# Kernel tuning notes

Hardware: AMD Instinct MI355X
Metric: run time of the kernel (lower is better)

The kernel has to match this reference:

```python
import jax, jax.numpy as jnp
import numpy as np

Z_SIZE, KEY_SIZE, HID = 128, 256, 512
NEG = -1e9


def setup_inputs() -> dict:
    key = jax.random.key(0)
    ks = jax.random.split(key, 8)
    B, T, H, W, Y = 512, 32, 32, 32, 4
    D = H * W
    g = lambda k, shape, s: jax.random.normal(k, shape, jnp.float32) * s
    return {
        "x_seq": jax.random.normal(ks[0], (B, T, H, W), jnp.float32),
        # Encoder (conv encoder stand-in: flatten -> MLP -> z_size)
        "enc_w1": g(ks[1], (D, HID), 0.03),
        "enc_b1": jnp.zeros((HID,), jnp.float32),
        "enc_w2": g(ks[2], (HID, Z_SIZE), 0.05),
        "enc_b2": jnp.zeros((Z_SIZE,), jnp.float32),
        # LSTM input kernel (recurrent kernel unused: h_prev is always 0)
        "lstm_Wx": g(ks[3], (KEY_SIZE + 1, 4 * HID), 0.05),
        "lstm_b": jnp.zeros((4 * HID,), jnp.float32),
        "keyw_W": g(ks[4], (HID, KEY_SIZE), 0.05),
        "keyw_b": jnp.zeros((KEY_SIZE,), jnp.float32),
        "g_W": g(ks[5], (HID, 1), 0.05),
        "g_b": jnp.zeros((1,), jnp.float32),
        "y_W": g(ks[6], (HID, Y), 0.05),
        "y_b": jnp.zeros((Y,), jnp.float32),
        "conf_gain": jnp.float32(1.0),
        "conf_bias": jnp.float32(0.0),
    }


def reference(x_seq, enc_w1, enc_b1, enc_w2, enc_b2, lstm_Wx, lstm_b,
              keyw_W, keyw_b, g_W, g_b, y_W, y_b, conf_gain, conf_bias):
    B, T = x_seq.shape[0], x_seq.shape[1]
    Y = y_b.shape[0]
    dt = x_seq.dtype

    # Encode all frames at once: (B, T, Z)
    x_flat = x_seq.reshape(B, T, -1)
    z_seq = jax.nn.relu(x_flat @ enc_w1 + enc_b1) @ enc_w2 + enc_b2
    # Pad with the zero z_t used at the final step t == T  -> (B, T+1, Z)
    z_pad = jnp.concatenate([z_seq, jnp.zeros((B, 1, Z_SIZE), dt)], axis=1)

    def lstm_step(x):  # single keras LSTM step from zero state (h=c=0)
        gates = x @ lstm_Wx + lstm_b
        i, f, c, o = jnp.split(gates, 4, axis=-1)  # keras gate order i,f,c,o
        c_new = jax.nn.sigmoid(i) * jnp.tanh(c)     # f*c_prev = 0
        return jax.nn.sigmoid(o) * jnp.tanh(c_new)

    slot_idx = jnp.arange(T + 1)

    def step(carry, t):
        key_r, M_k, M_v, _ = carry
        z_t = z_pad[:, t]                       # (B, Z)
        h = lstm_step(key_r)                    # (B, HID)
        key_w = h @ keyw_W + keyw_b             # (B, KEY)
        gate = jax.nn.sigmoid(h @ g_W + g_b)    # (B, 1)
        y_lin = h @ y_W + y_b                   # (B, Y)

        # Content-based read over memory slots written so far (slots < t)
        scores = jnp.einsum('bz,btz->bt', z_t, M_v)          # (B, T+1)
        valid = (slot_idx < t)[None, :]
        w_k = jax.nn.softmax(jnp.where(valid, scores, NEG), axis=1)
        c_k = jax.nn.sigmoid(scores * conf_gain + conf_bias)  # (B, T+1)
        Mkc = jnp.concatenate([M_k, c_k[..., None]], axis=-1)  # (B, T+1, KEY+1)
        key_r_new = gate * jnp.einsum('bt,btk->bk', w_k, Mkc)
        key_r_new = jnp.where(t == 0, jnp.zeros_like(key_r_new), key_r_new)

        # Memory write (append == write into preallocated slot t)
        M_k = M_k.at[:, t].set(key_w)
        M_v = M_v.at[:, t].set(z_t)
        return (key_r_new, M_k, M_v, y_lin), None

    init = (jnp.zeros((B, KEY_SIZE + 1), dt),
            jnp.zeros((B, T + 1, KEY_SIZE), dt),
            jnp.zeros((B, T + 1, Z_SIZE), dt),
            jnp.zeros((B, Y), dt))
    (_, _, _, y_pred_linear), _ = jax.lax.scan(step, init, jnp.arange(T + 1))
    y_pred = jnp.argmax(y_pred_linear, axis=1)
    return y_pred_linear, y_pred
```

## Files before the change

### kernel.cpp

```cpp
#include <hip/hip_runtime.h>
#include <math.h>

__device__ __forceinline__ float sigf(float x) { return 1.0f / (1.0f + expf(-x)); }
__device__ __forceinline__ float4 f4fma(float s, float4 b, float4 a) {
  return make_float4(fmaf(s, b.x, a.x), fmaf(s, b.y, a.y), fmaf(s, b.z, a.z), fmaf(s, b.w, a.w));
}
__device__ __forceinline__ void wave_red2(float4& v) {
  v.x += __shfl_xor(v.x, 16); v.y += __shfl_xor(v.y, 16);
  v.z += __shfl_xor(v.z, 16); v.w += __shfl_xor(v.w, 16);
  v.x += __shfl_xor(v.x, 32); v.y += __shfl_xor(v.y, 32);
  v.z += __shfl_xor(v.z, 32); v.w += __shfl_xor(v.w, 32);
}

__global__ __launch_bounds__(256) void k_gemm1(const float* __restrict__ X,
                                               const float* __restrict__ W,
                                               const float* __restrict__ Bv,
                                               float* __restrict__ C)
{
  const int K = 1024, N = 512;
  __shared__ float As[16][132];
  __shared__ float Bs[16][132];
  int tid = threadIdx.x;
  int bm = blockIdx.x >> 2;
  int bn = blockIdx.x & 3;
  int tx = tid & 15, ty = tid >> 4;
  int xr = tid & 127, xc8 = (tid >> 7) * 8;
  int wk = tid >> 4, wc = (tid & 15) * 8;
  const float* Xb = X + (size_t)(bm * 128 + xr) * K;
  const float* Wb = W + bn * 128 + wc;
  float acc[8][8];
#pragma unroll
  for (int i = 0; i < 8; i++)
#pragma unroll
    for (int j = 0; j < 8; j++) acc[i][j] = 0.f;

  for (int k0 = 0; k0 < K; k0 += 16) {
    float4 a0 = *(const float4*)(Xb + k0 + xc8);
    float4 a1 = *(const float4*)(Xb + k0 + xc8 + 4);
    float4 b0 = *(const float4*)(W + (size_t)(k0 + wk) * N + bn * 128 + wc);
    float4 b1 = *(const float4*)(W + (size_t)(k0 + wk) * N + bn * 128 + wc + 4);
    As[xc8 + 0][xr] = a0.x; As[xc8 + 1][xr] = a0.y;
    As[xc8 + 2][xr] = a0.z; As[xc8 + 3][xr] = a0.w;
    As[xc8 + 4][xr] = a1.x; As[xc8 + 5][xr] = a1.y;
    As[xc8 + 6][xr] = a1.z; As[xc8 + 7][xr] = a1.w;
    *(float4*)(&Bs[wk][wc]) = b0;
    *(float4*)(&Bs[wk][wc + 4]) = b1;
    __syncthreads();
#pragma unroll
    for (int kk = 0; kk < 16; kk++) {
      float a[8], b[8];
      *(float4*)(a)     = *(const float4*)(&As[kk][ty * 8]);
      *(float4*)(a + 4) = *(const float4*)(&As[kk][ty * 8 + 4]);
      *(float4*)(b)     = *(const float4*)(&Bs[kk][tx * 4]);
      *(float4*)(b + 4) = *(const float4*)(&Bs[kk][64 + tx * 4]);
#pragma unroll
      for (int i = 0; i < 8; i++)
#pragma unroll
        for (int j = 0; j < 8; j++) acc[i][j] = fmaf(a[i], b[j], acc[i][j]);
    }
    __syncthreads();
  }
  int crow0 = bm * 128 + ty * 8;
  int ccolA = bn * 128 + tx * 4;
  int ccolB = bn * 128 + 64 + tx * 4;
  float4 bvA = *(const float4*)(Bv + ccolA);
  float4 bvB = *(const float4*)(Bv + ccolB);
#pragma unroll
  for (int i = 0; i < 8; i++) {
    float4 vA = make_float4(acc[i][0] + bvA.x, acc[i][1] + bvA.y,
                            acc[i][2] + bvA.z, acc[i][3] + bvA.w);
    float4 vB = make_float4(acc[i][4] + bvB.x, acc[i][5] + bvB.y,
                            acc[i][6] + bvB.z, acc[i][7] + bvB.w);
    vA.x = vA.x > 0.f ? vA.x : 0.f; vA.y = vA.y > 0.f ? vA.y : 0.f;
    vA.z = vA.z > 0.f ? vA.z : 0.f; vA.w = vA.w > 0.f ? vA.w : 0.f;
    vB.x = vB.x > 0.f ? vB.x : 0.f; vB.y = vB.y > 0.f ? vB.y : 0.f;
    vB.z = vB.z > 0.f ? vB.z : 0.f; vB.w = vB.w > 0.f ? vB.w : 0.f;
    *(float4*)(&C[(size_t)(crow0 + i) * N + ccolA]) = vA;
    *(float4*)(&C[(size_t)(crow0 + i) * N + ccolB]) = vB;
  }
}

__global__ __launch_bounds__(256) void k_gemm2(const float* __restrict__ A,
                                               const float* __restrict__ W,
                                               const float* __restrict__ Bv,
                                               float* __restrict__ zp)
{
  const int K = 512, N = 128;
  __shared__ float As[8][132];
  __shared__ float Bs[8][132];
  int tid = threadIdx.x;
  int bm = blockIdx.x;
  int tx = tid & 15, ty = tid >> 4;
  int arow = tid >> 1, acol4 = (tid & 1) * 4;
  int bkk = tid >> 5, bn4 = (tid & 31) * 4;
  const float* Ab = A + (size_t)(bm * 128) * K;
  float acc[8][8];
#pragma unroll
  for (int i = 0; i < 8; i++)
#pragma unroll
    for (int j2 = 0; j2 < 8; j2++) acc[i][j2] = 0.f;
  for (int k0 = 0; k0 < K; k0 += 8) {
    float4 av = *(const float4*)(Ab + (size_t)arow * K + k0 + acol4);
    float4 bv = *(const float4*)(W + (size_t)(k0 + bkk) * N + bn4);
    As[acol4 + 0][arow] = av.x;
    As[acol4 + 1][arow] = av.y;
    As[acol4 + 2][arow] = av.z;
    As[acol4 + 3][arow] = av.w;
    *(float4*)(&Bs[bkk][bn4]) = bv;
    __syncthreads();
#pragma unroll
    for (int kk = 0; kk < 8; kk++) {
      float a[8], b[8];
      *(float4*)(a)     = *(const float4*)(&As[kk][ty * 8]);
      *(float4*)(a + 4) = *(const float4*)(&As[kk][ty * 8 + 4]);
      *(float4*)(b)     = *(const float4*)(&Bs[kk][tx * 8]);
      *(float4*)(b + 4) = *(const float4*)(&Bs[kk][tx * 8 + 4]);
#pragma unroll
      for (int i = 0; i < 8; i++)
#pragma unroll
        for (int j2 = 0; j2 < 8; j2++) acc[i][j2] = fmaf(a[i], b[j2], acc[i][j2]);
    }
    __syncthreads();
  }
  int ccol0 = tx * 8;
#pragma unroll
  for (int i = 0; i < 8; i++) {
    int r = bm * 128 + ty * 8 + i;
    int b = r >> 5, tt = r & 31;
#pragma unroll
    for (int j2 = 0; j2 < 8; j2++) {
      zp[(size_t)b * (33 * 128) + tt * 128 + ccol0 + j2] = acc[i][j2] + Bv[ccol0 + j2];
    }
  }
}

__global__ __launch_bounds__(256) void k_gram(const float* __restrict__ zp,
                                              float* __restrict__ warr,
                                              float* __restrict__ wc,
                                              const float* __restrict__ cgp,
                                              const float* __restrict__ cbp)
{
  __shared__ float zl[32][128];
  __shared__ float sg[32][32];
  int b = blockIdx.x, tid = threadIdx.x;
  const float* zb = zp + (size_t)b * (33 * 128);
  for (int i = tid; i < 32 * 128; i += 256) (&zl[0][0])[i] = zb[i];
  __syncthreads();
  for (int p = tid; p < 496; p += 256) {
    int t = 1;
    while (p >= t * (t + 1) / 2) t++;
    int tp = p - t * (t - 1) / 2;
    const float* za = &zl[t][0];
    const float* zc = &zl[tp][0];
    float s = 0.f;
#pragma unroll 4
    for (int c = 0; c < 128; c += 4) {
      s += za[c] * zc[c] + za[c + 1] * zc[c + 1] + za[c + 2] * zc[c + 2] + za[c + 3] * zc[c + 3];
    }
    sg[t][tp] = s;
  }
  __syncthreads();
  if (tid >= 1 && tid < 32) {
    int t = tid;
    float cg = cgp[0], cb = cbp[0];
    float m = -3.0e38f;
    for (int tp = 0; tp < t; tp++) m = fmaxf(m, sg[t][tp]);
    float se = 0.f;
    for (int tp = 0; tp < t; tp++) se += expf(sg[t][tp] - m);
    float inv = 1.0f / se;
    float wcs = 0.f;
    for (int tp = 0; tp < t; tp++) {
      float s = sg[t][tp];
      float w = expf(s - m) * inv;
      warr[(size_t)b * 1024 + t * 32 + tp] = w;
      wcs = fmaf(w, sigf(fmaf(s, cg, cb)), wcs);
    }
    wc[b * 32 + t] = wcs;
  }
}

__global__ __launch_bounds__(256) void k_gates(const float* __restrict__ Wx,
                                               const float* __restrict__ lb,
                                               const float* __restrict__ keyrT,
                                               float* __restrict__ h, int t)
{
  __shared__ float smem[6656];
  float* As = smem;
  float* Bs = smem + 640;
  float* Rb = smem;
  const int tid = threadIdx.x;
  const int rt = blockIdx.x >> 4;
  const int ct = blockIdx.x & 15;
  const int row0 = rt * 16;
  const int hc0 = ct * 32;

  if (t > 0) {
    const int ksub = tid >> 4;
    const int pos = tid & 15;
    const int rg = pos >> 3;
    const int cg = pos & 7;
    float4 aI[8], aC[8], aO[8];
#pragma unroll
    for (int r = 0; r < 8; r++) {
      aI[r] = make_float4(0.f, 0.f, 0.f, 0.f);
      aC[r] = make_float4(0.f, 0.f, 0.f, 0.f);
      aO[r] = make_float4(0.f, 0.f, 0.f, 0.f);
    }
    for (int c = 0; c < 8; ++c) {
      const int k0 = c * 32;
      if (c) __syncthreads();
      if (tid < 128) {
        const int kkA = tid >> 2, lA = (tid & 3) * 4;
        *(float4*)&As[kkA * 20 + lA] =
            *(const float4*)&keyrT[(size_t)(k0 + kkA) * 512 + row0 + lA];
      }
      {
        const int kkB = tid >> 3, lB = (tid & 7) * 4;
        const float* wrow = Wx + (size_t)(k0 + kkB) * 2048;
        *(float4*)&Bs[kkB * 100 + lB]      = *(const float4*)(wrow + hc0 + lB);
        *(float4*)&Bs[kkB * 100 + 32 + lB] = *(const float4*)(wrow + 1024 + hc0 + lB);
        *(float4*)&Bs[kkB * 100 + 64 + lB] = *(const float4*)(wrow + 1536 + hc0 + lB);
      }
      __syncthreads();
#pragma unroll
      for (int i = 0; i < 2; ++i) {
        const int kk = ksub * 2 + i;
        float a8[8];
        *(float4*)&a8[0] = *(const float4*)&As[kk * 20 + rg * 8];
        *(float4*)&a8[4] = *(const float4*)&As[kk * 20 + rg * 8 + 4];
        float4 bI = *(const float4*)&Bs[kk * 100 + cg * 4];
        float4 bC = *(const float4*)&Bs[kk * 100 + 32 + cg * 4];
        float4 bO = *(const float4*)&Bs[kk * 100 + 64 + cg * 4];
#pragma unroll
        for (int r = 0; r < 8; r++) {
          float a = a8[r];
          aI[r] = f4fma(a, bI, aI[r]);
          aC[r] = f4fma(a, bC, aC[r]);
          aO[r] = f4fma(a, bO, aO[r]);
        }
      }
    }
    if (ksub == 0) {
      float a8[8];
      *(float4*)&a8[0] = *(const float4*)&keyrT[(size_t)256 * 512 + row0 + rg * 8];
      *(float4*)&a8[4] = *(const float4*)&keyrT[(size_t)256 * 512 + row0 + rg * 8 + 4];
      const float* wrow = Wx + (size_t)256 * 2048;
      float4 bI = *(const float4*)(wrow + hc0 + cg * 4);
      float4 bC = *(const float4*)(wrow + 1024 + hc0 + cg * 4);
      float4 bO = *(const float4*)(wrow + 1536 + hc0 + cg * 4);
#pragma unroll
      for (int r = 0; r < 8; r++) {
        float a = a8[r];
        aI[r] = f4fma(a, bI, aI[r]);
        aC[r] = f4fma(a, bC, aC[r]);
        aO[r] = f4fma(a, bO, aO[r]);
      }
    }
#pragma unroll
    for (int r = 0; r < 8; r++) { wave_red2(aI[r]); wave_red2(aC[r]); wave_red2(aO[r]); }
    __syncthreads();
    {
      const int wave = tid >> 6, lane = tid & 63;
      if (lane < 16) {
        float* w = &Rb[wave * 1600 + lane * 100];
#pragma unroll
        for (int r = 0; r < 8; r++) {
          *(float4*)&w[r * 12 + 0] = aI[r];
          *(float4*)&w[r * 12 + 4] = aC[r];
          *(float4*)&w[r * 12 + 8] = aO[r];
        }
      }
    }
    __syncthreads();
    {
      const int r = tid >> 4;
      const int hc2 = (tid & 15) * 2;
      const int p = (r >> 3) * 8 + (hc2 >> 2);
      const int base = p * 100 + (r & 7) * 12;
      const int off = hc2 & 3;
      float sI0 = Rb[base + off]     + Rb[1600 + base + off]     + Rb[3200 + base + off]     + Rb[4800 + base + off];
      float sI1 = Rb[base + off + 1] + Rb[1600 + base + off + 1] + Rb[3200 + base + off + 1] + Rb[4800 + base + off + 1];
      float sC0 = Rb[base + 4 + off]     + Rb[1600 + base + 4 + off]     + Rb[3200 + base + 4 + off]     + Rb[4800 + base + 4 + off];
      float sC1 = Rb[base + 4 + off + 1] + Rb[1600 + base + 4 + off + 1] + Rb[3200 + base + 4 + off + 1] + Rb[4800 + base + 4 + off + 1];
      float sO0 = Rb[base + 8 + off]     + Rb[1600 + base + 8 + off]     + Rb[3200 + base + 8 + off]     + Rb[4800 + base + 8 + off];
      float sO1 = Rb[base + 8 + off + 1] + Rb[1600 + base + 8 + off + 1] + Rb[3200 + base + 8 + off + 1] + Rb[4800 + base + 8 + off + 1];
      float iv0 = sI0 + lb[hc0 + hc2],        iv1 = sI1 + lb[hc0 + hc2 + 1];
      float cv0 = sC0 + lb[1024 + hc0 + hc2], cv1 = sC1 + lb[1024 + hc0 + hc2 + 1];
      float ov0 = sO0 + lb[1536 + hc0 + hc2], ov1 = sO1 + lb[1536 + hc0 + hc2 + 1];
      float h0 = sigf(ov0) * tanhf(sigf(iv0) * tanhf(cv0));
      float h1 = sigf(ov1) * tanhf(sigf(iv1) * tanhf(cv1));
      *(float2*)&h[(size_t)(row0 + r) * 512 + hc0 + hc2] = make_float2(h0, h1);
    }
  } else {
    const int r = tid >> 4;
    const int hc2 = (tid & 15) * 2;
    float iv0 = lb[hc0 + hc2],        iv1 = lb[hc0 + hc2 + 1];
    float cv0 = lb[1024 + hc0 + hc2], cv1 = lb[1024 + hc0 + hc2 + 1];
    float ov0 = lb[1536 + hc0 + hc2], ov1 = lb[1536 + hc0 + hc2 + 1];
    float h0 = sigf(ov0) * tanhf(sigf(iv0) * tanhf(cv0));
    float h1 = sigf(ov1) * tanhf(sigf(iv1) * tanhf(cv1));
    *(float2*)&h[(size_t)(row0 + r) * 512 + hc0 + hc2] = make_float2(h0, h1);
  }
}

__global__ __launch_bounds__(256) void k_update(const float* __restrict__ h,
                                                const float* __restrict__ kW,
                                                const float* __restrict__ kb,
                                                const float* __restrict__ gW,
                                                const float* __restrict__ gb,
                                                const float* __restrict__ warr,
                                                const float* __restrict__ wc,
                                                float* __restrict__ Mk,
                                                float* __restrict__ keyrT, int t)
{
  __shared__ float smem[10640];
  float* hs  = smem;
  float* gWs = smem + 8256;
  float* wws = smem + 8768;
  float* gsh = smem + 9344;
  float* kWs = smem + 9360;
  float* Rb  = smem + 9360;
  const int tid = threadIdx.x;
  const int rt = blockIdx.x >> 4;
  const int ct = blockIdx.x & 15;
  const int row0 = rt * 16;
  const int c0 = ct * 16;

  {
    const int r = tid >> 4, seg = tid & 15;
    const float* hrow = h + (size_t)(row0 + r) * 512 + seg * 32;
    float* hd = hs + r * 516 + seg * 32;
#pragma unroll
    for (int q = 0; q < 8; ++q) {
      const int qp = ((q + seg) & 7) * 4;
      *(float4*)&hd[qp] = *(const float4*)&hrow[qp];
    }
    if (tid < 128) *(float4*)&gWs[tid * 4] = *(const float4*)&gW[tid * 4];
    wws[r * 36 + seg]      = (seg < t)      ? warr[(size_t)(row0 + r) * 1024 + t * 32 + seg] : 0.f;
    wws[r * 36 + 16 + seg] = (16 + seg < t) ? warr[(size_t)(row0 + r) * 1024 + t * 32 + 16 + seg] : 0.f;
  }
  __syncthreads();

  const int ksub = tid >> 4, pu = tid & 15, rgu = pu >> 2, cgu = pu & 3;
  float4 au[4];
#pragma unroll
  for (int r = 0; r < 4; r++) au[r] = make_float4(0.f, 0.f, 0.f, 0.f);
  for (int c = 0; c < 16; ++c) {
    if (c) __syncthreads();
    if (tid < 128) {
      const int kkW = tid >> 2, lW = (tid & 3) * 4;
      *(float4*)&kWs[kkW * 20 + lW] =
          *(const float4*)&kW[(size_t)(c * 32 + kkW) * 256 + c0 + lW];
    }
    __syncthreads();
#pragma unroll
    for (int i = 0; i < 2; ++i) {
      const int kk = ksub * 2 + i;
      float4 b4 = *(const float4*)&kWs[kk * 20 + cgu * 4];
      const int kidx = c * 32 + kk;
#pragma unroll
      for (int jj = 0; jj < 4; ++jj) {
        float a = hs[(rgu * 4 + jj) * 516 + kidx];
        au[jj] = f4fma(a, b4, au[jj]);
      }
    }
  }
#pragma unroll
  for (int r = 0; r < 4; r++) wave_red2(au[r]);
  __syncthreads();
  {
    const int wave = tid >> 6, lane = tid & 63;
    if (lane < 16) {
      float* w = &Rb[wave * 320 + lane * 20];
#pragma unroll
      for (int r = 0; r < 4; r++) *(float4*)&w[r * 4] = au[r];
    }
  }
  __syncthreads();
  {
    const int r = tid >> 4, cc = tid & 15;
    const int p = (r >> 2) * 4 + (cc >> 2);
    const int e = p * 20 + (r & 3) * 4 + (cc & 3);
    float v = Rb[e] + Rb[320 + e] + Rb[640 + e] + Rb[960 + e];
    Mk[(size_t)(row0 + r) * 8192 + t * 256 + c0 + cc] = v + kb[c0 + cc];
  }
  {
    const int r = tid >> 4, seg = tid & 15;
    const float* hp = &hs[r * 516 + seg * 32];
    const float* gp = &gWs[seg * 32];
    float s = 0.f;
#pragma unroll 8
    for (int j = 0; j < 32; ++j) s = fmaf(hp[j], gp[j], s);
    s += __shfl_xor(s, 1); s += __shfl_xor(s, 2);
    s += __shfl_xor(s, 4); s += __shfl_xor(s, 8);
    if (seg == 0) gsh[r] = sigf(s + gb[0]);
  }
  __syncthreads();
  {
    const int r = tid >> 4, cc = tid & 15;
    const int row = row0 + r;
    if (t == 0) {
      keyrT[(size_t)(c0 + cc) * 512 + row] = 0.f;
      if (ct == 0 && cc == 0) keyrT[(size_t)256 * 512 + row] = 0.f;
    } else {
      float a = 0.f;
      const float* mkb = Mk + (size_t)row * 8192 + c0 + cc;
      const float* wp = &wws[r * 36];
      for (int tp = 0; tp < t; ++tp) a = fmaf(wp[tp], mkb[tp * 256], a);
      float g = gsh[r];
      keyrT[(size_t)(c0 + cc) * 512 + row] = g * a;
      if (ct == 0 && cc == 0)
        keyrT[(size_t)256 * 512 + row] = g * wc[row * 32 + t];
    }
  }
}

__global__ __launch_bounds__(256) void k_y(const float* __restrict__ h,
                                           const float* __restrict__ yW,
                                           const float* __restrict__ yb,
                                           float* __restrict__ out)
{
  int tid = threadIdx.x;
  int wave = tid >> 6, lane = tid & 63;
  int row = blockIdx.x * 4 + wave;
  float a0 = 0.f, a1 = 0.f, a2 = 0.f, a3 = 0.f;
  for (int k = lane; k < 512; k += 64) {
    float hv = h[(size_t)row * 512 + k];
    float4 w4 = *(const float4*)(yW + k * 4);
    a0 = fmaf(hv, w4.x, a0);
    a1 = fmaf(hv, w4.y, a1);
    a2 = fmaf(hv, w4.z, a2);
    a3 = fmaf(hv, w4.w, a3);
  }
#pragma unroll
  for (int off = 32; off > 0; off >>= 1) {
    a0 += __shfl_xor(a0, off);
    a1 += __shfl_xor(a1, off);
    a2 += __shfl_xor(a2, off);
    a3 += __shfl_xor(a3, off);
  }
  if (lane == 0) {
    a0 += yb[0]; a1 += yb[1]; a2 += yb[2]; a3 += yb[3];
    out[row * 4 + 0] = a0;
    out[row * 4 + 1] = a1;
    out[row * 4 + 2] = a2;
    out[row * 4 + 3] = a3;
    int bi = 0; float bv = a0;
    if (a1 > bv) { bv = a1; bi = 1; }
    if (a2 > bv) { bv = a2; bi = 2; }
    if (a3 > bv) { bv = a3; bi = 3; }
    out[2048 + row] = (float)bi;
  }
}

extern "C" void kernel_launch(void* const* d_in, const int* in_sizes, int n_in,
                              void* d_out, int out_size, void* d_ws, size_t ws_size,
                              hipStream_t stream)
{
  const float* x  = (const float*)d_in[0];
  const float* w1 = (const float*)d_in[1];
  const float* b1 = (const float*)d_in[2];
  const float* w2 = (const float*)d_in[3];
  const float* b2 = (const float*)d_in[4];
  const float* Wx = (const float*)d_in[5];
  const float* lb = (const float*)d_in[6];
  const float* kW = (const float*)d_in[7];
  const float* kb = (const float*)d_in[8];
  const float* gW = (const float*)d_in[9];
  const float* gb = (const float*)d_in[10];
  const float* yW = (const float*)d_in[11];
  const float* yb = (const float*)d_in[12];
  const float* cg = (const float*)d_in[13];
  const float* cb = (const float*)d_in[14];
  float* out = (float*)d_out;
  char* ws = (char*)d_ws;
  float* C1    = (float*)(ws);
  float* Mk    = (float*)(ws);
  float* warr  = (float*)(ws + 16777216);
  float* wcb   = (float*)(ws + 18874368);
  float* keyrT = (float*)(ws + 18939904);
  float* h     = (float*)(ws + 19466240);
  float* zp    = (float*)(ws + 33554432);

  hipLaunchKernelGGL(k_gemm1, dim3(512), dim3(256), 0, stream, x, w1, b1, C1);
  hipLaunchKernelGGL(k_gemm2, dim3(128), dim3(256), 0, stream, C1, w2, b2, zp);
  hipLaunchKernelGGL(k_gram, dim3(512), dim3(256), 0, stream, zp, warr, wcb, cg, cb);
  for (int t = 0; t <= 32; t++) {
    hipLaunchKernelGGL(k_gates, dim3(512), dim3(256), 0, stream, Wx, lb, keyrT, h, t);
    if (t < 32) {
      hipLaunchKernelGGL(k_update, dim3(512), dim3(256), 0, stream,
                         h, kW, kb, gW, gb, warr, wcb, Mk, keyrT, t);
    }
  }
  hipLaunchKernelGGL(k_y, dim3(128), dim3(256), 0, stream, h, yW, yb, out);
}
```

Baseline: 1.320 ms.

## Fuse per-step gate and memory-update kernels into one split-K step kernel with atomics

Merges the LSTM gate kernel and the memory-update kernel into a single per-timestep kernel, halving launches in the recurrent loop. The key-write projection is split across column tiles and accumulated with atomicAdd into Mk and a gate accumulator, and the gated read is deferred to the next step through double-buffered partial buffers. The encoder GEMMs also get smaller tiles so more blocks are launched. The cost is float atomics with nondeterministic summation order, extra initialisation of Mk and gacc, and more complex cross-step dependencies.

```diff
diff --git a/kernel.cpp b/kernel.cpp
--- a/kernel.cpp
+++ b/kernel.cpp
@@ -18,63 +18,65 @@
                                                float* __restrict__ C)
 {
   const int K = 1024, N = 512;
-  __shared__ float As[16][132];
+  __shared__ float As[16][68];
   __shared__ float Bs[16][132];
-  int tid = threadIdx.x;
-  int bm = blockIdx.x >> 2;
-  int bn = blockIdx.x & 3;
-  int tx = tid & 15, ty = tid >> 4;
-  int xr = tid & 127, xc8 = (tid >> 7) * 8;
-  int wk = tid >> 4, wc = (tid & 15) * 8;
-  const float* Xb = X + (size_t)(bm * 128 + xr) * K;
-  const float* Wb = W + bn * 128 + wc;
-  float acc[8][8];
-#pragma unroll
-  for (int i = 0; i < 8; i++)
+  const int tid = threadIdx.x;
+  const int bm = blockIdx.x >> 2;
+  const int bn = blockIdx.x & 3;
+  const int ty = tid >> 4, tx = tid & 15;
+  const int ar = tid & 63, ac4 = (tid >> 6) * 4;
+  const int bk = tid >> 4, bc8 = (tid & 15) * 8;
+  const float* Xb = X + (size_t)(bm * 64 + ar) * K;
+  float acc[4][8];
+#pragma unroll
+  for (int i = 0; i < 4; i++)
 #pragma unroll
     for (int j = 0; j < 8; j++) acc[i][j] = 0.f;
 
   for (int k0 = 0; k0 < K; k0 += 16) {
-    float4 a0 = *(const float4*)(Xb + k0 + xc8);
-    float4 a1 = *(const float4*)(Xb + k0 + xc8 + 4);
-    float4 b0 = *(const float4*)(W + (size_t)(k0 + wk) * N + bn * 128 + wc);
-    float4 b1 = *(const float4*)(W + (size_t)(k0 + wk) * N + bn * 128 + wc + 4);
-    As[xc8 + 0][xr] = a0.x; As[xc8 + 1][xr] = a0.y;
-    As[xc8 + 2][xr] = a0.z; As[xc8 + 3][xr] = a0.w;
-    As[xc8 + 4][xr] = a1.x; As[xc8 + 5][xr] = a1.y;
-    As[xc8 + 6][xr] = a1.z; As[xc8 + 7][xr] = a1.w;
-    *(float4*)(&Bs[wk][wc]) = b0;
-    *(float4*)(&Bs[wk][wc + 4]) = b1;
+    float4 av = *(const float4*)(Xb + k0 + ac4);
+    float4 b0 = *(const float4*)(W + (size_t)(k0 + bk) * N + bn * 128 + bc8);
+    float4 b1 = *(const float4*)(W + (size_t)(k0 + bk) * N + bn * 128 + bc8 + 4);
+    As[ac4 + 0][ar] = av.x; As[ac4 + 1][ar] = av.y;
+    As[ac4 + 2][ar] = av.z; As[ac4 + 3][ar] = av.w;
+    *(float4*)(&Bs[bk][bc8]) = b0;
+    *(float4*)(&Bs[bk][bc8 + 4]) = b1;
     __syncthreads();
 #pragma unroll
     for (int kk = 0; kk < 16; kk++) {
-      float a[8], b[8];
-      *(float4*)(a)     = *(const float4*)(&As[kk][ty * 8]);
-      *(float4*)(a + 4) = *(const float4*)(&As[kk][ty * 8 + 4]);
-      *(float4*)(b)     = *(const float4*)(&Bs[kk][tx * 4]);
-      *(float4*)(b + 4) = *(const float4*)(&Bs[kk][64 + tx * 4]);
-#pragma unroll
-      for (int i = 0; i < 8; i++)
-#pragma unroll
-        for (int j = 0; j < 8; j++) acc[i][j] = fmaf(a[i], b[j], acc[i][j]);
-    }
-    __syncthreads();
-  }
-  int crow0 = bm * 128 + ty * 8;
-  int ccolA = bn * 128 + tx * 4;
-  int ccolB = bn * 128 + 64 + tx * 4;
+      float4 a = *(const float4*)(&As[kk][ty * 4]);
+      float4 bA = *(const float4*)(&Bs[kk][tx * 4]);
+      float4 bB = *(const float4*)(&Bs[kk][64 + tx * 4]);
+      float ar4[4] = {a.x, a.y, a.z, a.w};
+#pragma unroll
+      for (int i = 0; i < 4; i++) {
+        acc[i][0] = fmaf(ar4[i], bA.x, acc[i][0]);
+        acc[i][1] = fmaf(ar4[i], bA.y, acc[i][1]);
+        acc[i][2] = fmaf(ar4[i], bA.z, acc[i][2]);
+        acc[i][3] = fmaf(ar4[i], bA.w, acc[i][3]);
+        acc[i][4] = fmaf(ar4[i], bB.x, acc[i][4]);
+        acc[i][5] = fmaf(ar4[i], bB.y, acc[i][5]);
+        acc[i][6] = fmaf(ar4[i], bB.z, acc[i][6]);
+        acc[i][7] = fmaf(ar4[i], bB.w, acc[i][7]);
+      }
+    }
+    __syncthreads();
+  }
+  const int crow0 = bm * 64 + ty * 4;
+  const int ccolA = bn * 128 + tx * 4;
+  const int ccolB = ccolA + 64;
   float4 bvA = *(const float4*)(Bv + ccolA);
   float4 bvB = *(const float4*)(Bv + ccolB);
 #pragma unroll
-  for (int i = 0; i < 8; i++) {
+  for (int i = 0; i < 4; i++) {
     float4 vA = make_float4(acc[i][0] + bvA.x, acc[i][1] + bvA.y,
                             acc[i][2] + bvA.z, acc[i][3] + bvA.w);
     float4 vB = make_float4(acc[i][4] + bvB.x, acc[i][5] + bvB.y,
                             acc[i][6] + bvB.z, acc[i][7] + bvB.w);
-    vA.x = vA.x > 0.f ? vA.x : 0.f; vA.y = vA.y > 0.f ? vA.y : 0.f;
-    vA.z = vA.z > 0.f ? vA.z : 0.f; vA.w = vA.w > 0.f ? vA.w : 0.f;
-    vB.x = vB.x > 0.f ? vB.x : 0.f; vB.y = vB.y > 0.f ? vB.y : 0.f;
-    vB.z = vB.z > 0.f ? vB.z : 0.f; vB.w = vB.w > 0.f ? vB.w : 0.f;
+    vA.x = fmaxf(vA.x, 0.f); vA.y = fmaxf(vA.y, 0.f);
+    vA.z = fmaxf(vA.z, 0.f); vA.w = fmaxf(vA.w, 0.f);
+    vB.x = fmaxf(vB.x, 0.f); vB.y = fmaxf(vB.y, 0.f);
+    vB.z = fmaxf(vB.z, 0.f); vB.w = fmaxf(vB.w, 0.f);
     *(float4*)(&C[(size_t)(crow0 + i) * N + ccolA]) = vA;
     *(float4*)(&C[(size_t)(crow0 + i) * N + ccolB]) = vB;
   }
@@ -86,51 +88,57 @@
                                                float* __restrict__ zp)
 {
   const int K = 512, N = 128;
-  __shared__ float As[8][132];
-  __shared__ float Bs[8][132];
-  int tid = threadIdx.x;
-  int bm = blockIdx.x;
-  int tx = tid & 15, ty = tid >> 4;
-  int arow = tid >> 1, acol4 = (tid & 1) * 4;
-  int bkk = tid >> 5, bn4 = (tid & 31) * 4;
-  const float* Ab = A + (size_t)(bm * 128) * K;
-  float acc[8][8];
-#pragma unroll
-  for (int i = 0; i < 8; i++)
-#pragma unroll
-    for (int j2 = 0; j2 < 8; j2++) acc[i][j2] = 0.f;
-  for (int k0 = 0; k0 < K; k0 += 8) {
-    float4 av = *(const float4*)(Ab + (size_t)arow * K + k0 + acol4);
-    float4 bv = *(const float4*)(W + (size_t)(k0 + bkk) * N + bn4);
-    As[acol4 + 0][arow] = av.x;
-    As[acol4 + 1][arow] = av.y;
-    As[acol4 + 2][arow] = av.z;
-    As[acol4 + 3][arow] = av.w;
-    *(float4*)(&Bs[bkk][bn4]) = bv;
-    __syncthreads();
-#pragma unroll
-    for (int kk = 0; kk < 8; kk++) {
-      float a[8], b[8];
-      *(float4*)(a)     = *(const float4*)(&As[kk][ty * 8]);
-      *(float4*)(a + 4) = *(const float4*)(&As[kk][ty * 8 + 4]);
-      *(float4*)(b)     = *(const float4*)(&Bs[kk][tx * 8]);
-      *(float4*)(b + 4) = *(const float4*)(&Bs[kk][tx * 8 + 4]);
-#pragma unroll
-      for (int i = 0; i < 8; i++)
-#pragma unroll
-        for (int j2 = 0; j2 < 8; j2++) acc[i][j2] = fmaf(a[i], b[j2], acc[i][j2]);
-    }
-    __syncthreads();
-  }
-  int ccol0 = tx * 8;
-#pragma unroll
-  for (int i = 0; i < 8; i++) {
-    int r = bm * 128 + ty * 8 + i;
+  __shared__ float As[16][36];
+  __shared__ float Bs[16][132];
+  const int tid = threadIdx.x;
+  const int bm = blockIdx.x;
+  const int ty = tid >> 4, tx = tid & 15;
+  const int ar = tid & 31, ac4 = ((tid >> 5) & 3) * 4;
+  const int bk = tid >> 4, bc8 = (tid & 15) * 8;
+  float acc[2][8];
+#pragma unroll
+  for (int i = 0; i < 2; i++)
+#pragma unroll
+    for (int j = 0; j < 8; j++) acc[i][j] = 0.f;
+
+  for (int k0 = 0; k0 < K; k0 += 16) {
+    if (tid < 128) {
+      float4 av = *(const float4*)(A + (size_t)(bm * 32 + ar) * K + k0 + ac4);
+      As[ac4 + 0][ar] = av.x; As[ac4 + 1][ar] = av.y;
+      As[ac4 + 2][ar] = av.z; As[ac4 + 3][ar] = av.w;
+    }
+    *(float4*)(&Bs[bk][bc8]) = *(const float4*)(W + (size_t)(k0 + bk) * N + bc8);
+    *(float4*)(&Bs[bk][bc8 + 4]) = *(const float4*)(W + (size_t)(k0 + bk) * N + bc8 + 4);
+    __syncthreads();
+#pragma unroll
+    for (int kk = 0; kk < 16; kk++) {
+      float a0 = As[kk][ty * 2], a1 = As[kk][ty * 2 + 1];
+      float4 bA = *(const float4*)(&Bs[kk][tx * 4]);
+      float4 bB = *(const float4*)(&Bs[kk][64 + tx * 4]);
+      acc[0][0] = fmaf(a0, bA.x, acc[0][0]); acc[0][1] = fmaf(a0, bA.y, acc[0][1]);
+      acc[0][2] = fmaf(a0, bA.z, acc[0][2]); acc[0][3] = fmaf(a0, bA.w, acc[0][3]);
+      acc[0][4] = fmaf(a0, bB.x, acc[0][4]); acc[0][5] = fmaf(a0, bB.y, acc[0][5]);
+      acc[0][6] = fmaf(a0, bB.z, acc[0][6]); acc[0][7] = fmaf(a0, bB.w, acc[0][7]);
+      acc[1][0] = fmaf(a1, bA.x, acc[1][0]); acc[1][1] = fmaf(a1, bA.y, acc[1][1]);
+      acc[1][2] = fmaf(a1, bA.z, acc[1][2]); acc[1][3] = fmaf(a1, bA.w, acc[1][3]);
+      acc[1][4] = fmaf(a1, bB.x, acc[1][4]); acc[1][5] = fmaf(a1, bB.y, acc[1][5]);
+      acc[1][6] = fmaf(a1, bB.z, acc[1][6]); acc[1][7] = fmaf(a1, bB.w, acc[1][7]);
+    }
+    __syncthreads();
+  }
+  const int ccolA = tx * 4, ccolB = ccolA + 64;
+  float4 bvA = *(const float4*)(Bv + ccolA);
+  float4 bvB = *(const float4*)(Bv + ccolB);
+#pragma unroll
+  for (int i = 0; i < 2; i++) {
+    int r = bm * 32 + ty * 2 + i;
     int b = r >> 5, tt = r & 31;
-#pragma unroll
-    for (int j2 = 0; j2 < 8; j2++) {
-      zp[(size_t)b * (33 * 128) + tt * 128 + ccol0 + j2] = acc[i][j2] + Bv[ccol0 + j2];
-    }
+    float4 vA = make_float4(acc[i][0] + bvA.x, acc[i][1] + bvA.y,
+                            acc[i][2] + bvA.z, acc[i][3] + bvA.w);
+    float4 vB = make_float4(acc[i][4] + bvB.x, acc[i][5] + bvB.y,
+                            acc[i][6] + bvB.z, acc[i][7] + bvB.w);
+    *(float4*)(&zp[(size_t)b * 4096 + tt * 128 + ccolA]) = vA;
+    *(float4*)(&zp[(size_t)b * 4096 + tt * 128 + ccolB]) = vB;
   }
 }
 
@@ -138,13 +146,18 @@
                                               float* __restrict__ warr,
                                               float* __restrict__ wc,
                                               const float* __restrict__ cgp,
-                                              const float* __restrict__ cbp)
+                                              const float* __restrict__ cbp,
+                                              const float* __restrict__ kb,
+                                              float* __restrict__ Mk,
+                                              float* __restrict__ gacc)
 {
   __shared__ float zl[32][128];
   __shared__ float sg[32][32];
   int b = blockIdx.x, tid = threadIdx.x;
-  const float* zb = zp + (size_t)b * (33 * 128);
+  const float* zb = zp + (size_t)b * 4096;
   for (int i = tid; i < 32 * 128; i += 256) (&zl[0][0])[i] = zb[i];
+  Mk[(size_t)b * 8192 + tid] = kb[tid];
+  if (tid == 0) gacc[b * 32] = 0.f;
   __syncthreads();
   for (int p = tid; p < 496; p += 256) {
     int t = 1;
@@ -179,22 +192,47 @@
   }
 }
 
-__global__ __launch_bounds__(256) void k_gates(const float* __restrict__ Wx,
-                                               const float* __restrict__ lb,
-                                               const float* __restrict__ keyrT,
-                                               float* __restrict__ h, int t)
-{
-  __shared__ float smem[6656];
-  float* As = smem;
-  float* Bs = smem + 640;
-  float* Rb = smem;
+__global__ __launch_bounds__(256) void k_step(
+    const float* __restrict__ Wx, const float* __restrict__ lb,
+    const float* __restrict__ kW, const float* __restrict__ kb,
+    const float* __restrict__ gW, const float* __restrict__ gb,
+    const float* __restrict__ warr, const float* __restrict__ wc,
+    float* __restrict__ Mk, float* __restrict__ gacc,
+    const float* __restrict__ Pr, float* __restrict__ Pw,
+    float* __restrict__ h, int t)
+{
+  __shared__ float smem[9984];
+  float* As   = smem;
+  float* Bs   = smem + 5140;
+  float* Rb   = smem;
+  float* kWs  = smem;
+  float* hs   = smem + 8340;
+  float* wws  = smem + 8916;
+  float* gt16 = smem + 9428;
+  float* gsh  = smem + 9684;
+  float* Ptmp = smem + 9700;
   const int tid = threadIdx.x;
   const int rt = blockIdx.x >> 4;
   const int ct = blockIdx.x & 15;
   const int row0 = rt * 16;
   const int hc0 = ct * 32;
-
-  if (t > 0) {
+  const int c0 = ct * 16;
+
+  if (t >= 2) {
+    if (tid < 16) gsh[tid] = sigf(gacc[(row0 + tid) * 32 + (t - 1)] + gb[0]);
+    __syncthreads();
+    const int p16 = tid >> 4, r16 = tid & 15;
+    const float g = gsh[r16];
+#pragma unroll 4
+    for (int kg = 0; kg < 16; ++kg) {
+      const int k = kg * 16 + p16;
+      As[k * 20 + r16] = g * Pr[(size_t)k * 512 + row0 + r16];
+    }
+    if (p16 == 0) As[256 * 20 + r16] = g * wc[(row0 + r16) * 32 + (t - 1)];
+    __syncthreads();
+  }
+
+  if (t >= 2) {
     const int ksub = tid >> 4;
     const int pos = tid & 15;
     const int rg = pos >> 3;
@@ -207,16 +245,10 @@
       aO[r] = make_float4(0.f, 0.f, 0.f, 0.f);
     }
     for (int c = 0; c < 8; ++c) {
-      const int k0 = c * 32;
       if (c) __syncthreads();
-      if (tid < 128) {
-        const int kkA = tid >> 2, lA = (tid & 3) * 4;
-        *(float4*)&As[kkA * 20 + lA] =
-            *(const float4*)&keyrT[(size_t)(k0 + kkA) * 512 + row0 + lA];
-      }
       {
         const int kkB = tid >> 3, lB = (tid & 7) * 4;
-        const float* wrow = Wx + (size_t)(k0 + kkB) * 2048;
+        const float* wrow = Wx + (size_t)(c * 32 + kkB) * 2048;
         *(float4*)&Bs[kkB * 100 + lB]      = *(const float4*)(wrow + hc0 + lB);
         *(float4*)&Bs[kkB * 100 + 32 + lB] = *(const float4*)(wrow + 1024 + hc0 + lB);
         *(float4*)&Bs[kkB * 100 + 64 + lB] = *(const float4*)(wrow + 1536 + hc0 + lB);
@@ -225,9 +257,10 @@
 #pragma unroll
       for (int i = 0; i < 2; ++i) {
         const int kk = ksub * 2 + i;
+        const int kabs = c * 32 + kk;
         float a8[8];
-        *(float4*)&a8[0] = *(const float4*)&As[kk * 20 + rg * 8];
-        *(float4*)&a8[4] = *(const float4*)&As[kk * 20 + rg * 8 + 4];
+        *(float4*)&a8[0] = *(const float4*)&As[kabs * 20 + rg * 8];
+        *(float4*)&a8[4] = *(const float4*)&As[kabs * 20 + rg * 8 + 4];
         float4 bI = *(const float4*)&Bs[kk * 100 + cg * 4];
         float4 bC = *(const float4*)&Bs[kk * 100 + 32 + cg * 4];
         float4 bO = *(const float4*)&Bs[kk * 100 + 64 + cg * 4];
@@ -242,8 +275,8 @@
     }
     if (ksub == 0) {
       float a8[8];
-      *(float4*)&a8[0] = *(const float4*)&keyrT[(size_t)256 * 512 + row0 + rg * 8];
-      *(float4*)&a8[4] = *(const float4*)&keyrT[(size_t)256 * 512 + row0 + rg * 8 + 4];
+      *(float4*)&a8[0] = *(const float4*)&As[256 * 20 + rg * 8];
+      *(float4*)&a8[4] = *(const float4*)&As[256 * 20 + rg * 8 + 4];
       const float* wrow = Wx + (size_t)256 * 2048;
       float4 bI = *(const float4*)(wrow + hc0 + cg * 4);
       float4 bC = *(const float4*)(wrow + 1024 + hc0 + cg * 4);
@@ -289,128 +322,96 @@
       float ov0 = sO0 + lb[1536 + hc0 + hc2], ov1 = sO1 + lb[1536 + hc0 + hc2 + 1];
       float h0 = sigf(ov0) * tanhf(sigf(iv0) * tanhf(cv0));
       float h1 = sigf(ov1) * tanhf(sigf(iv1) * tanhf(cv1));
-      *(float2*)&h[(size_t)(row0 + r) * 512 + hc0 + hc2] = make_float2(h0, h1);
+      hs[r * 36 + hc2] = h0;
+      hs[r * 36 + hc2 + 1] = h1;
+      if (t == 32) *(float2*)&h[(size_t)(row0 + r) * 512 + hc0 + hc2] = make_float2(h0, h1);
     }
   } else {
     const int r = tid >> 4;
     const int hc2 = (tid & 15) * 2;
-    float iv0 = lb[hc0 + hc2],        iv1 = lb[hc0 + hc2 + 1];
-    float cv0 = lb[1024 + hc0 + hc2], cv1 = lb[1024 + hc0 + hc2 + 1];
-    float ov0 = lb[1536 + hc0 + hc2], ov1 = lb[1536 + hc0 + hc2 + 1];
-    float h0 = sigf(ov0) * tanhf(sigf(iv0) * tanhf(cv0));
-    float h1 = sigf(ov1) * tanhf(sigf(iv1) * tanhf(cv1));
-    *(float2*)&h[(size_t)(row0 + r) * 512 + hc0 + hc2] = make_float2(h0, h1);
-  }
-}
-
-__global__ __launch_bounds__(256) void k_update(const float* __restrict__ h,
-                                                const float* __restrict__ kW,
-                                                const float* __restrict__ kb,
-                                                const float* __restrict__ gW,
-                                                const float* __restrict__ gb,
-                                                const float* __restrict__ warr,
-                                                const float* __restrict__ wc,
-                                                float* __restrict__ Mk,
-                                                float* __restrict__ keyrT, int t)
-{
-  __shared__ float smem[10640];
-  float* hs  = smem;
-  float* gWs = smem + 8256;
-  float* wws = smem + 8768;
-  float* gsh = smem + 9344;
-  float* kWs = smem + 9360;
-  float* Rb  = smem + 9360;
-  const int tid = threadIdx.x;
-  const int rt = blockIdx.x >> 4;
-  const int ct = blockIdx.x & 15;
-  const int row0 = rt * 16;
-  const int c0 = ct * 16;
-
-  {
-    const int r = tid >> 4, seg = tid & 15;
-    const float* hrow = h + (size_t)(row0 + r) * 512 + seg * 32;
-    float* hd = hs + r * 516 + seg * 32;
-#pragma unroll
-    for (int q = 0; q < 8; ++q) {
-      const int qp = ((q + seg) & 7) * 4;
-      *(float4*)&hd[qp] = *(const float4*)&hrow[qp];
-    }
-    if (tid < 128) *(float4*)&gWs[tid * 4] = *(const float4*)&gW[tid * 4];
-    wws[r * 36 + seg]      = (seg < t)      ? warr[(size_t)(row0 + r) * 1024 + t * 32 + seg] : 0.f;
-    wws[r * 36 + 16 + seg] = (16 + seg < t) ? warr[(size_t)(row0 + r) * 1024 + t * 32 + 16 + seg] : 0.f;
+    float h0 = sigf(lb[1536 + hc0 + hc2])     * tanhf(sigf(lb[hc0 + hc2])     * tanhf(lb[1024 + hc0 + hc2]));
+    float h1 = sigf(lb[1536 + hc0 + hc2 + 1]) * tanhf(sigf(lb[hc0 + hc2 + 1]) * tanhf(lb[1024 + hc0 + hc2 + 1]));
+    hs[r * 36 + hc2] = h0;
+    hs[r * 36 + hc2 + 1] = h1;
   }
   __syncthreads();
 
-  const int ksub = tid >> 4, pu = tid & 15, rgu = pu >> 2, cgu = pu & 3;
-  float4 au[4];
-#pragma unroll
-  for (int r = 0; r < 4; r++) au[r] = make_float4(0.f, 0.f, 0.f, 0.f);
-  for (int c = 0; c < 16; ++c) {
-    if (c) __syncthreads();
-    if (tid < 128) {
-      const int kkW = tid >> 2, lW = (tid & 3) * 4;
-      *(float4*)&kWs[kkW * 20 + lW] =
-          *(const float4*)&kW[(size_t)(c * 32 + kkW) * 256 + c0 + lW];
-    }
-    __syncthreads();
-#pragma unroll
-    for (int i = 0; i < 2; ++i) {
-      const int kk = ksub * 2 + i;
-      float4 b4 = *(const float4*)&kWs[kk * 20 + cgu * 4];
-      const int kidx = c * 32 + kk;
-#pragma unroll
-      for (int jj = 0; jj < 4; ++jj) {
-        float a = hs[(rgu * 4 + jj) * 516 + kidx];
-        au[jj] = f4fma(a, b4, au[jj]);
-      }
-    }
-  }
-#pragma unroll
-  for (int r = 0; r < 4; r++) wave_red2(au[r]);
-  __syncthreads();
-  {
-    const int wave = tid >> 6, lane = tid & 63;
-    if (lane < 16) {
-      float* w = &Rb[wave * 320 + lane * 20];
-#pragma unroll
-      for (int r = 0; r < 4; r++) *(float4*)&w[r * 4] = au[r];
-    }
-  }
-  __syncthreads();
-  {
-    const int r = tid >> 4, cc = tid & 15;
-    const int p = (r >> 2) * 4 + (cc >> 2);
-    const int e = p * 20 + (r & 3) * 4 + (cc & 3);
-    float v = Rb[e] + Rb[320 + e] + Rb[640 + e] + Rb[960 + e];
-    Mk[(size_t)(row0 + r) * 8192 + t * 256 + c0 + cc] = v + kb[c0 + cc];
-  }
-  {
-    const int r = tid >> 4, seg = tid & 15;
-    const float* hp = &hs[r * 516 + seg * 32];
-    const float* gp = &gWs[seg * 32];
-    float s = 0.f;
-#pragma unroll 8
-    for (int j = 0; j < 32; ++j) s = fmaf(hp[j], gp[j], s);
-    s += __shfl_xor(s, 1); s += __shfl_xor(s, 2);
-    s += __shfl_xor(s, 4); s += __shfl_xor(s, 8);
-    if (seg == 0) gsh[r] = sigf(s + gb[0]);
-  }
-  __syncthreads();
-  {
-    const int r = tid >> 4, cc = tid & 15;
-    const int row = row0 + r;
-    if (t == 0) {
-      keyrT[(size_t)(c0 + cc) * 512 + row] = 0.f;
-      if (ct == 0 && cc == 0) keyrT[(size_t)256 * 512 + row] = 0.f;
-    } else {
-      float a = 0.f;
-      const float* mkb = Mk + (size_t)row * 8192 + c0 + cc;
-      const float* wp = &wws[r * 36];
-      for (int tp = 0; tp < t; ++tp) a = fmaf(wp[tp], mkb[tp * 256], a);
-      float g = gsh[r];
-      keyrT[(size_t)(c0 + cc) * 512 + row] = g * a;
-      if (ct == 0 && cc == 0)
-        keyrT[(size_t)256 * 512 + row] = g * wc[row * 32 + t];
+  if (t < 32) {
+    const int rC = tid >> 4, cb = tid & 15;
+    float4 a16[4];
+#pragma unroll
+    for (int j = 0; j < 4; j++) a16[j] = make_float4(0.f, 0.f, 0.f, 0.f);
+#pragma unroll
+    for (int half = 0; half < 2; ++half) {
+      __syncthreads();
+      {
+        const int rowW = tid >> 4;
+        const int cc4 = (tid & 15) * 4;
+#pragma unroll
+        for (int q = 0; q < 4; ++q) {
+          *(float4*)&kWs[rowW * 260 + cc4 + q * 64] =
+              *(const float4*)&kW[(size_t)(hc0 + half * 16 + rowW) * 256 + cc4 + q * 64];
+        }
+      }
+      __syncthreads();
+#pragma unroll
+      for (int kk = 0; kk < 16; ++kk) {
+        float a = hs[rC * 36 + half * 16 + kk];
+#pragma unroll
+        for (int j = 0; j < 4; ++j) {
+          float4 b = *(const float4*)&kWs[kk * 260 + j * 64 + cb * 4];
+          a16[j] = f4fma(a, b, a16[j]);
+        }
+      }
+    }
+    {
+      float* mkt = Mk + (size_t)(row0 + rC) * 8192 + t * 256;
+#pragma unroll
+      for (int j = 0; j < 4; ++j) {
+        atomicAdd(&mkt[j * 64 + cb * 4 + 0], a16[j].x);
+        atomicAdd(&mkt[j * 64 + cb * 4 + 1], a16[j].y);
+        atomicAdd(&mkt[j * 64 + cb * 4 + 2], a16[j].z);
+        atomicAdd(&mkt[j * 64 + cb * 4 + 3], a16[j].w);
+      }
+    }
+    {
+      float gs = hs[rC * 36 + cb * 2] * gW[hc0 + cb * 2] +
+                 hs[rC * 36 + cb * 2 + 1] * gW[hc0 + cb * 2 + 1];
+      gt16[rC * 16 + cb] = gs;
+    }
+    __syncthreads();
+    if (tid < 16) {
+      float s = 0.f;
+#pragma unroll
+      for (int p = 0; p < 16; ++p) s += gt16[tid * 16 + p];
+      atomicAdd(&gacc[(row0 + tid) * 32 + t], s);
+    }
+
+    if (t < 31) {
+      const int rD = tid >> 4, cD = tid & 15;
+      Mk[(size_t)(row0 + rD) * 8192 + (t + 1) * 256 + c0 + cD] = kb[c0 + cD];
+      if (ct == 0 && tid < 16) gacc[(row0 + tid) * 32 + (t + 1)] = 0.f;
+    }
+    if (t >= 1) {
+      {
+        const int r = tid >> 4, s = tid & 15;
+        wws[r * 32 + s]      = (s < t)      ? warr[(size_t)(row0 + r) * 1024 + t * 32 + s] : 0.f;
+        wws[r * 32 + 16 + s] = (16 + s < t) ? warr[(size_t)(row0 + r) * 1024 + t * 32 + 16 + s] : 0.f;
+      }
+      __syncthreads();
+      {
+        const int rD = tid >> 4, cD = tid & 15;
+        const float* mkb = Mk + (size_t)(row0 + rD) * 8192 + c0 + cD;
+        const float* wp = &wws[rD * 32];
+        float acc = 0.f;
+        for (int tp = 0; tp < t; ++tp) acc = fmaf(wp[tp], mkb[tp * 256], acc);
+        Ptmp[cD * 17 + rD] = acc;
+      }
+      __syncthreads();
+      {
+        const int cW = tid >> 4, rW = tid & 15;
+        Pw[(size_t)(c0 + cW) * 512 + row0 + rW] = Ptmp[cW * 17 + rW];
+      }
     }
   }
 }
@@ -474,23 +475,24 @@
   const float* cb = (const float*)d_in[14];
   float* out = (float*)d_out;
   char* ws = (char*)d_ws;
-  float* C1    = (float*)(ws);
-  float* Mk    = (float*)(ws);
-  float* warr  = (float*)(ws + 16777216);
-  float* wcb   = (float*)(ws + 18874368);
-  float* keyrT = (float*)(ws + 18939904);
-  float* h     = (float*)(ws + 19466240);
-  float* zp    = (float*)(ws + 33554432);
-
-  hipLaunchKernelGGL(k_gemm1, dim3(512), dim3(256), 0, stream, x, w1, b1, C1);
-  hipLaunchKernelGGL(k_gemm2, dim3(128), dim3(256), 0, stream, C1, w2, b2, zp);
-  hipLaunchKernelGGL(k_gram, dim3(512), dim3(256), 0, stream, zp, warr, wcb, cg, cb);
+  float* C1   = (float*)(ws);
+  float* Mk   = (float*)(ws);
+  float* warr = (float*)(ws + 16777216);
+  float* wcb  = (float*)(ws + 18874368);
+  float* gacc = (float*)(ws + 18939904);
+  float* P0   = (float*)(ws + 19005440);
+  float* P1   = (float*)(ws + 19529728);
+  float* h    = (float*)(ws + 20054016);
+  float* zp   = (float*)(ws + 33554432);
+
+  hipLaunchKernelGGL(k_gemm1, dim3(1024), dim3(256), 0, stream, x, w1, b1, C1);
+  hipLaunchKernelGGL(k_gemm2, dim3(512), dim3(256), 0, stream, C1, w2, b2, zp);
+  hipLaunchKernelGGL(k_gram, dim3(512), dim3(256), 0, stream, zp, warr, wcb, cg, cb, kb, Mk, gacc);
   for (int t = 0; t <= 32; t++) {
-    hipLaunchKernelGGL(k_gates, dim3(512), dim3(256), 0, stream, Wx, lb, keyrT, h, t);
-    if (t < 32) {
-      hipLaunchKernelGGL(k_update, dim3(512), dim3(256), 0, stream,
-                         h, kW, kb, gW, gb, warr, wcb, Mk, keyrT, t);
-    }
+    float* Pr = (t & 1) ? P1 : P0;
+    float* Pw = ((t + 1) & 1) ? P1 : P0;
+    hipLaunchKernelGGL(k_step, dim3(512), dim3(256), 0, stream,
+                       Wx, lb, kW, kb, gW, gb, warr, wcb, Mk, gacc, Pr, Pw, h, t);
   }
   hipLaunchKernelGGL(k_y, dim3(128), dim3(256), 0, stream, h, yW, yb, out);
 }
```

After: 1.817 ms. 1.38x slower.
